# Optimization experiments

Measured on AMD Instinct MI355X. Metric: run time of the kernel, lower is better.

The kernel has to match this reference:

```python
import jax, jax.numpy as jnp
import numpy as np

B, S, D, H = 128, 512, 512, 4
DH = D // H

def setup_inputs() -> dict:
    key = jax.random.key(0)
    ks = jax.random.split(key, 12)
    s = 1.0 / np.sqrt(D)
    inp = {
        "x": jax.random.normal(ks[0], (B, S, D), dtype=jnp.float32),
        "Wi": jax.random.uniform(ks[1], (D, D), jnp.float32, -s, s),
        "bi": jnp.zeros((D,), jnp.float32),
        "Wq": jax.random.uniform(ks[2], (D, D), jnp.float32, -s, s),
        "bq": jnp.zeros((D,), jnp.float32),
        "Wk": jax.random.uniform(ks[3], (D, D), jnp.float32, -s, s),
        "bk": jnp.zeros((D,), jnp.float32),
        "Wv": jax.random.uniform(ks[4], (D, D), jnp.float32, -s, s),
        "bv": jnp.zeros((D,), jnp.float32),
        "Wo": jax.random.uniform(ks[5], (D, D), jnp.float32, -s, s),
        "bo": jnp.zeros((D,), jnp.float32),
        "data_lens": jax.random.randint(ks[6], (B,), 1, S + 1, dtype=jnp.int32),
    }
    return inp


def _forward(x, Wi, bi, Wq, bq, Wk, bk, Wv, bv, Wo, bo, data_lens):
    # fc_i applied to the whole sequence up front
    xf = x @ Wi + bi                      # [B, S, D]
    h0 = xf[:, 0, :]                      # initial state = fc_i(x)[:, 0]
    scale = 1.0 / jnp.sqrt(jnp.asarray(DH, xf.dtype))

    def step(h, x_t):
        # h: [B, D] previous state (acts as key and value, kv_len == 1)
        # x_t: [B, D] current input (query)
        q = (x_t @ Wq + bq).reshape(B, H, DH)
        k = (h @ Wk + bk).reshape(B, H, DH)
        v = (h @ Wv + bv).reshape(B, H, DH)
        scores = jnp.sum(q * k, axis=-1, keepdims=True) * scale   # [B, H, 1]
        w = jax.nn.softmax(scores, axis=-1)                       # == 1 (single key)
        attn = (w * v).reshape(B, D)
        h_new = attn @ Wo + bo + x_t                              # residual
        return h_new, h_new

    xs = jnp.transpose(xf, (1, 0, 2))     # [S, B, D]
    _, outs = jax.lax.scan(step, h0, xs)  # [S, B, D]
    outputs = jnp.transpose(outs, (1, 0, 2))                      # [B, S, D]

    idx = (data_lens.astype(jnp.int32) - 1)[:, None, None]        # [B,1,1]
    final_state = jnp.take_along_axis(outputs, idx, axis=1)[:, 0, :]
    return outputs, final_state


def reference(x, Wi, bi, Wq, bq, Wk, bk, Wv, bv, Wo, bo, data_lens):
    return _forward(x, Wi, bi, Wq, bq, Wk, bk, Wv, bv, Wo, bo, data_lens)
```

## Files before the change

kernel.cpp:

```cpp
#include <hip/hip_runtime.h>
#include <hip/hip_bf16.h>

typedef __hip_bfloat16 bf16;
typedef __attribute__((ext_vector_type(8))) short short8;
typedef __attribute__((ext_vector_type(4))) float f32x4;

#define S_LEN 512
#define DIM   512
#define BATCH 128
#define ROWS  (BATCH * S_LEN)

__device__ inline unsigned short f2bu(float f){
    bf16 h = __float2bfloat16(f);
    return *reinterpret_cast<unsigned short*>(&h);
}
__device__ inline float ld_in(const void* p, size_t i, int f32){
    return f32 ? ((const float*)p)[i] : __bfloat162float(((const bf16*)p)[i]);
}

typedef __attribute__((address_space(1))) const unsigned int gu32;
typedef __attribute__((address_space(3))) unsigned int lu32;
__device__ __forceinline__ void gld16(const void* g, void* l){
    __builtin_amdgcn_global_load_lds((gu32*)g, (lu32*)l, 16, 0, 0);
}

__global__ void detect_dtype(const unsigned int* __restrict__ x, int* __restrict__ flag)
{
    __shared__ int cnt;
    if (threadIdx.x == 0) cnt = 0;
    __syncthreads();
    int loc = 0;
    for (int i = threadIdx.x; i < 8192; i += 256)
        if (((x[i] >> 7) & 0xFFu) == 0xFFu) loc++;
    atomicAdd(&cnt, loc);
    __syncthreads();
    if (threadIdx.x == 0) *flag = (cnt > 0) ? 1 : 0;
}

__global__ void conv_tr(const void* __restrict__ in, bf16* __restrict__ outp,
                        const int* __restrict__ flagp)
{
    const int f32 = *flagp;
    __shared__ unsigned short tile[32][33];
    const int bx = blockIdx.x, by = blockIdx.y;
    const int tx = threadIdx.x, ty = threadIdx.y;
    #pragma unroll
    for (int j = 0; j < 32; j += 8)
        tile[ty + j][tx] = f2bu(ld_in(in, (size_t)(by*32 + ty + j)*DIM + bx*32 + tx, f32));
    __syncthreads();
    #pragma unroll
    for (int j = 0; j < 32; j += 8) {
        unsigned short u = tile[tx][ty + j];
        outp[(size_t)(bx*32 + ty + j)*DIM + by*32 + tx] = *reinterpret_cast<bf16*>(&u);
    }
}

__global__ void conv_cp(const void* __restrict__ in, bf16* __restrict__ outp,
                        const int* __restrict__ flagp)
{
    const int f32 = *flagp;
    const size_t i = (size_t)blockIdx.x*256 + threadIdx.x;
    outp[i] = __float2bfloat16(ld_in(in, i, f32));
}

__global__ void conv_x(const void* __restrict__ X, size_t eoff, bf16* __restrict__ xb,
                       const int* __restrict__ flagp)
{
    const int f32 = *flagp;
    const size_t i = ((size_t)blockIdx.x*256 + threadIdx.x)*8;
    if (f32) {
        const float* p = (const float*)X + eoff + i;
        float4 a = *(const float4*)p;
        float4 b = *(const float4*)(p + 4);
        __align__(16) unsigned short wv[8];
        wv[0]=f2bu(a.x); wv[1]=f2bu(a.y); wv[2]=f2bu(a.z); wv[3]=f2bu(a.w);
        wv[4]=f2bu(b.x); wv[5]=f2bu(b.y); wv[6]=f2bu(b.z); wv[7]=f2bu(b.w);
        *(uint4*)(xb + i) = *(const uint4*)wv;
    } else {
        *(uint4*)(xb + i) = *(const uint4*)((const bf16*)X + eoff + i);
    }
}

__global__ void cvec_kernel(const bf16* __restrict__ WoT, const void* __restrict__ bv,
                            const void* __restrict__ bo, const void* __restrict__ bi,
                            const int* __restrict__ flagp,
                            float* __restrict__ dvec, float* __restrict__ bvec)
{
    const int f32 = *flagp;
    const int n = blockIdx.x * 4 + (threadIdx.x >> 6);
    const int lane = threadIdx.x & 63;
    float acc = 0.f;
    for (int k = lane; k < DIM; k += 64)
        acc += ld_in(bv, k, f32) * __bfloat162float(WoT[(size_t)n*DIM + k]);
    #pragma unroll
    for (int o = 32; o > 0; o >>= 1) acc += __shfl_down(acc, o, 64);
    if (lane == 0) {
        const float dd = acc + ld_in(bo, n, f32);
        dvec[n] = dd;
        bvec[n] = dd + ld_in(bi, n, f32);
    }
}

__global__ void prep_aux(const float* __restrict__ U0, const float* __restrict__ V0,
                         const float* __restrict__ dvec,
                         bf16* __restrict__ A1, bf16* __restrict__ V0b, bf16* __restrict__ Zr)
{
    const int idx = blockIdx.x * 256 + threadIdx.x;
    const int n = idx & 511;
    A1[idx]  = __float2bfloat16(U0[idx] - dvec[n]);
    V0b[idx] = __float2bfloat16(V0[idx]);
    if (idx < 512) Zr[idx] = __float2bfloat16(0.f);
}

#define TILE_PROLOGUE                                                          \
    __shared__ __align__(16) unsigned short As[128][72];                       \
    __shared__ __align__(16) unsigned short Bs[128][72];                       \
    const int tid  = threadIdx.x;                                              \
    const int lane = tid & 63;                                                 \
    const int wave = tid >> 6;                                                 \
    const int wm = (wave & 1) * 64;                                            \
    const int wn = (wave >> 1) * 64;                                           \
    const int cn = lane & 15;                                                  \
    const int quad = lane >> 4;                                                \
    f32x4 acc[4][4];                                                           \
    _Pragma("unroll")                                                          \
    for (int i = 0; i < 4; ++i)                                                \
        _Pragma("unroll")                                                      \
        for (int j = 0; j < 4; ++j) acc[i][j] = (f32x4){0.f,0.f,0.f,0.f};

#define TILE_MFMA                                                              \
        __syncthreads();                                                       \
        _Pragma("unroll")                                                      \
        for (int ks = 0; ks < 64; ks += 32) {                                  \
            short8 af[4], bfr[4];                                              \
            const int koff = ks + quad*8;                                      \
            _Pragma("unroll")                                                  \
            for (int i = 0; i < 4; ++i) af[i]  = *(const short8*)&As[wm + i*16 + cn][koff]; \
            _Pragma("unroll")                                                  \
            for (int j = 0; j < 4; ++j) bfr[j] = *(const short8*)&Bs[wn + j*16 + cn][koff]; \
            _Pragma("unroll")                                                  \
            for (int i = 0; i < 4; ++i)                                        \
                _Pragma("unroll")                                              \
                for (int j = 0; j < 4; ++j)                                    \
                    acc[i][j] = __builtin_amdgcn_mfma_f32_16x16x32_bf16(af[i], bfr[j], acc[i][j], 0, 0, 0); \
        }                                                                      \
        __syncthreads();

#define STAGE_B(Bt, C0)                                                        \
        {                                                                      \
            int r = tid >> 3; const int c = (tid & 7) * 8;                     \
            _Pragma("unroll")                                                  \
            for (int p = 0; p < 4; ++p, r += 32) {                             \
                uint4 v = *(const uint4*)((Bt) + (size_t)((C0) + r)*DIM + k0 + c); \
                *(uint4*)&Bs[r][c] = v;                                        \
            }                                                                  \
        }

#define STAGE_A_IN(SRC, BASE)                                                  \
                if (f32) {                                                     \
                    const float* sp = (const float*)(SRC) + (BASE);            \
                    float4 a = *(const float4*)sp;                             \
                    float4 b = *(const float4*)(sp + 4);                       \
                    __align__(16) unsigned short w[8];                         \
                    w[0]=f2bu(a.x); w[1]=f2bu(a.y); w[2]=f2bu(a.z); w[3]=f2bu(a.w); \
                    w[4]=f2bu(b.x); w[5]=f2bu(b.y); w[6]=f2bu(b.z); w[7]=f2bu(b.w); \
                    *(uint4*)&As[r][c] = *(const uint4*)w;                     \
                } else {                                                       \
                    *(uint4*)&As[r][c] = *(const uint4*)((const bf16*)(SRC) + (BASE)); \
                }

__global__ __launch_bounds__(256) void gemm_sq(const bf16* __restrict__ A,
        const bf16* __restrict__ Btm, bf16* __restrict__ Pout, bf16* __restrict__ Tout)
{
    TILE_PROLOGUE
    const int R0 = blockIdx.y * 128;
    const int C0 = blockIdx.x * 128;
    for (int k0 = 0; k0 < DIM; k0 += 64) {
        {
            int r = tid >> 3; const int c = (tid & 7) * 8;
            #pragma unroll
            for (int p = 0; p < 4; ++p, r += 32)
                *(uint4*)&As[r][c] = *(const uint4*)(A + (size_t)(R0 + r)*DIM + k0 + c);
        }
        STAGE_B(Btm, C0)
        TILE_MFMA
    }
    #pragma unroll
    for (int i = 0; i < 4; ++i) {
        const int rowb = R0 + wm + i*16 + quad*4;
        #pragma unroll
        for (int j = 0; j < 4; ++j) {
            const int cc = C0 + wn + j*16 + cn;
            #pragma unroll
            for (int rr = 0; rr < 4; ++rr) {
                const float v = acc[i][j][rr];
                Pout[(size_t)(rowb + rr)*DIM + cc] = __float2bfloat16(v);
                Tout[(size_t)cc*DIM + rowb + rr]  = __float2bfloat16(v);
            }
        }
    }
}

__global__ __launch_bounds__(256) void gemm_row0(const void* __restrict__ X,
        const bf16* __restrict__ WiT, const float* __restrict__ bvec,
        const int* __restrict__ flagp, float* __restrict__ U0)
{
    const int f32 = *flagp;
    TILE_PROLOGUE
    const int C0 = blockIdx.x * 128;
    for (int k0 = 0; k0 < DIM; k0 += 64) {
        {
            int r = tid >> 3; const int c = (tid & 7) * 8;
            #pragma unroll
            for (int p = 0; p < 4; ++p, r += 32) {
                const size_t base = (size_t)r*S_LEN*DIM + k0 + c;
                STAGE_A_IN(X, base)
            }
        }
        STAGE_B(WiT, C0)
        TILE_MFMA
    }
    #pragma unroll
    for (int i = 0; i < 4; ++i) {
        const int rowb = wm + i*16 + quad*4;
        #pragma unroll
        for (int j = 0; j < 4; ++j) {
            const int cc = C0 + wn + j*16 + cn;
            const float bb = bvec[cc];
            #pragma unroll
            for (int rr = 0; rr < 4; ++rr)
                U0[(size_t)(rowb + rr)*DIM + cc] = acc[i][j][rr] + bb;
        }
    }
}

__global__ __launch_bounds__(256) void gemm_v0(const float* __restrict__ U0,
        const bf16* __restrict__ T0, const float* __restrict__ dvec, float* __restrict__ V0)
{
    TILE_PROLOGUE
    const int C0 = blockIdx.x * 128;
    for (int k0 = 0; k0 < DIM; k0 += 64) {
        {
            int r = tid >> 3; const int c = (tid & 7) * 8;
            #pragma unroll
            for (int p = 0; p < 4; ++p, r += 32) {
                __align__(16) unsigned short w[8];
                #pragma unroll
                for (int q = 0; q < 8; ++q)
                    w[q] = f2bu(U0[(size_t)r*DIM + k0 + c + q] - dvec[k0 + c + q]);
                *(uint4*)&As[r][c] = *(const uint4*)w;
            }
        }
        STAGE_B(T0, C0)
        TILE_MFMA
    }
    #pragma unroll
    for (int i = 0; i < 4; ++i) {
        const int rowb = wm + i*16 + quad*4;
        #pragma unroll
        for (int j = 0; j < 4; ++j) {
            const int cc = C0 + wn + j*16 + cn;
            #pragma unroll
            for (int rr = 0; rr < 4; ++rr) {
                const size_t off = (size_t)(rowb + rr)*DIM + cc;
                V0[off] = acc[i][j][rr] + U0[off];
            }
        }
    }
}

template<int MODE, bool TO_OUT>
__global__ __launch_bounds__(256) void gemm_big(
        const bf16* __restrict__ Abf, const bf16* __restrict__ A1,
        const bf16* __restrict__ V0b, const bf16* __restrict__ Zr,
        const bf16* __restrict__ Bt,  const float* __restrict__ Rf,
        float* __restrict__ Of, bf16* __restrict__ Ob,
        void* __restrict__ Oout, size_t eoff, const int* __restrict__ flagp,
        const int shift)
{
    __shared__ __align__(16) unsigned short As[128*64];
    __shared__ __align__(16) unsigned short Bs[128*64];
    const int tid  = threadIdx.x;
    const int lane = tid & 63;
    const int w    = tid >> 6;
    const int nb = gridDim.x;
    const int p0 = blockIdx.x;
    const int L  = (p0 & 7) * (nb >> 3) + (p0 >> 3);
    const int bx = L & 3, by = L >> 2;
    const int R0 = by * 128, C0 = bx * 128;
    const int wm = (w & 1) * 64;
    const int wn = (w >> 1) * 64;
    const int cn = lane & 15;
    const int quad = lane >> 4;
    f32x4 acc[4][4];
    #pragma unroll
    for (int i = 0; i < 4; ++i)
        #pragma unroll
        for (int j = 0; j < 4; ++j) acc[i][j] = (f32x4){0.f,0.f,0.f,0.f};

    const int lr = lane >> 3;
    const int lc = (lane & 7) * 8;
    const bf16* ab[4];
    const bf16* bb[4];
    #pragma unroll
    for (int p = 0; p < 4; ++p) {
        const int seg  = w*4 + p;
        const int r    = seg*8 + lr;
        const int grow = R0 + r;
        const bf16* a;
        if (MODE == 2) {
            a = Abf + (size_t)grow*DIM;
        } else if (MODE == 1) {
            const int t = grow & (S_LEN - 1);
            if      (t == 0) a = A1  + (size_t)(grow >> 9)*DIM;
            else if (t == 1) a = V0b + (size_t)(grow >> 9)*DIM;
            else             a = Abf + (size_t)(grow - 1)*DIM;
        } else {
            const int t = grow & (S_LEN - 1);
            a = (t >= shift) ? (Abf + (size_t)(grow - shift)*DIM) : Zr;
        }
        ab[p] = a + lc;
        bb[p] = Bt + (size_t)(C0 + r)*DIM + lc;
    }

    for (int k0 = 0; k0 < DIM; k0 += 64) {
        #pragma unroll
        for (int p = 0; p < 4; ++p) {
            const int seg = w*4 + p;
            gld16(ab[p] + k0, &As[seg*512]);
            gld16(bb[p] + k0, &Bs[seg*512]);
        }
        __syncthreads();
        #pragma unroll
        for (int ks = 0; ks < 64; ks += 32) {
            short8 af[4], bfr[4];
            const int koff = ks + quad*8;
            #pragma unroll
            for (int i = 0; i < 4; ++i) af[i]  = *(const short8*)&As[(wm + i*16 + cn)*64 + koff];
            #pragma unroll
            for (int j = 0; j < 4; ++j) bfr[j] = *(const short8*)&Bs[(wn + j*16 + cn)*64 + koff];
            #pragma unroll
            for (int i = 0; i < 4; ++i)
                #pragma unroll
                for (int j = 0; j < 4; ++j)
                    acc[i][j] = __builtin_amdgcn_mfma_f32_16x16x32_bf16(af[i], bfr[j], acc[i][j], 0, 0, 0);
        }
        __syncthreads();
    }

    const int f32o = TO_OUT ? *flagp : 0;
    #pragma unroll
    for (int i = 0; i < 4; ++i) {
        const int rowb = R0 + wm + i*16 + quad*4;
        #pragma unroll
        for (int j = 0; j < 4; ++j) {
            const int cc = C0 + wn + j*16 + cn;
            #pragma unroll
            for (int rr = 0; rr < 4; ++rr) {
                const size_t off = (size_t)(rowb + rr)*DIM + cc;
                const float res = (MODE == 2) ? Rf[cc] : Rf[off];
                const float v = acc[i][j][rr] + res;
                if (TO_OUT) {
                    if (f32o) ((float*)Oout)[eoff + off] = v;
                    else      ((bf16*)Oout)[eoff + off]  = __float2bfloat16(v);
                } else {
                    Of[off] = v;
                    Ob[off] = __float2bfloat16(v);
                }
            }
        }
    }
}

__global__ void gather_final(void* __restrict__ out, const int* __restrict__ lens,
                             const int* __restrict__ flagp)
{
    const int f32 = *flagp;
    const int idx = blockIdx.x * 256 + threadIdx.x;
    const int b = idx >> 9, n = idx & 511;
    int L = lens[b];
    if (L < 1) L = 1;
    if (L > S_LEN) L = S_LEN;
    const size_t src = ((size_t)b*S_LEN + (L - 1))*DIM + n;
    const size_t dst = (size_t)ROWS*DIM + idx;
    if (f32) ((float*)out)[dst] = ((const float*)out)[src];
    else     ((bf16*)out)[dst]  = ((const bf16*)out)[src];
}

extern "C" void kernel_launch(void* const* d_in, const int* in_sizes, int n_in,
                              void* d_out, int out_size, void* d_ws, size_t ws_size,
                              hipStream_t stream)
{
    const void* X  = d_in[0];
    const void* Wi = d_in[1];
    const void* bi = d_in[2];
    const void* Wv = d_in[7];
    const void* bv = d_in[8];
    const void* Wo = d_in[9];
    const void* bo = d_in[10];
    const int* lens = (const int*)d_in[11];
    char* ws = (char*)d_ws;

    const size_t MATB = (size_t)DIM * DIM * sizeof(bf16);
    bf16* WiT = (bf16*)(ws + 0*MATB);
    bf16* WoT = (bf16*)(ws + 1*MATB);
    bf16* Wvb = (bf16*)(ws + 2*MATB);
    bf16* S2  = (bf16*)(ws + 3*MATB);
    bf16* S3  = (bf16*)(ws + 4*MATB);
    bf16* T0  = (bf16*)(ws + 5*MATB);
    bf16* T1  = (bf16*)(ws + 6*MATB);
    bf16* T2  = (bf16*)(ws + 7*MATB);
    bf16* T3  = (bf16*)(ws + 8*MATB);
    size_t off = 9*MATB;
    float* dvec = (float*)(ws + off); off += 2048;
    float* bvec = (float*)(ws + off); off += 2048;
    int*   flag = (int*)  (ws + off); off += 256;
    float* U0   = (float*)(ws + off); off += (size_t)BATCH*DIM*4;
    float* V0   = (float*)(ws + off); off += (size_t)BATCH*DIM*4;
    bf16*  A1   = (bf16*) (ws + off); off += (size_t)BATCH*DIM*2;
    bf16*  V0b  = (bf16*) (ws + off); off += (size_t)BATCH*DIM*2;
    bf16*  Zr   = (bf16*) (ws + off); off += 1024;
    off = (off + 1023) & ~(size_t)1023;
    char* dyn = ws + off;
    const size_t avail = ws_size > off ? ws_size - off : 0;

    int CR = 512;
    for (long cr = 65536; cr >= 512; cr >>= 1)
        if ((size_t)cr * 7168 <= avail) { CR = (int)cr; break; }

    bf16*  xbf = (bf16*) dyn;
    float* Uf  = (float*)(dyn + (size_t)CR*1024);
    bf16*  Ub  = (bf16*) (dyn + (size_t)CR*3072);
    float* Vf  = (float*)(dyn + (size_t)CR*4096);
    bf16*  Vb  = (bf16*) (dyn + (size_t)CR*6144);

    detect_dtype<<<1, 256, 0, stream>>>((const unsigned int*)X, flag);
    conv_tr<<<dim3(16,16), dim3(32,8), 0, stream>>>(Wi, WiT, flag);
    conv_tr<<<dim3(16,16), dim3(32,8), 0, stream>>>(Wo, WoT, flag);
    conv_cp<<<1024, 256, 0, stream>>>(Wv, Wvb, flag);
    cvec_kernel<<<128, 256, 0, stream>>>(WoT, bv, bo, bi, flag, dvec, bvec);
    gemm_sq<<<dim3(4,4), 256, 0, stream>>>(Wvb, WoT, S2, T0);
    gemm_sq<<<dim3(4,4), 256, 0, stream>>>(S2, T0, S3, T1);
    gemm_sq<<<dim3(4,4), 256, 0, stream>>>(S3, T1, S2, T2);
    gemm_sq<<<dim3(4,4), 256, 0, stream>>>(S2, T2, S3, T3);
    gemm_row0<<<dim3(4,1), 256, 0, stream>>>(X, WiT, bvec, flag, U0);
    gemm_v0<<<dim3(4,1), 256, 0, stream>>>(U0, T0, dvec, V0);
    prep_aux<<<256, 256, 0, stream>>>(U0, V0, dvec, A1, V0b, Zr);

    const int NC = ROWS / CR;
    const int RT = CR / 128;
    const int nb = 4 * RT;
    for (int c = 0; c < NC; ++c) {
        const size_t eoff = (size_t)c*CR*DIM;
        const size_t boff = (size_t)(c*(CR/S_LEN))*DIM;
        conv_x<<<CR/4, 256, 0, stream>>>(X, eoff, xbf, flag);
        gemm_big<2,false><<<nb, 256, 0, stream>>>(xbf, nullptr, nullptr, Zr,
                WiT, bvec, Uf, Ub, nullptr, 0, flag, 0);
        gemm_big<1,false><<<nb, 256, 0, stream>>>(Ub, A1 + boff, V0b + boff, Zr,
                T0, Uf, Vf, Vb, nullptr, 0, flag, 1);
        gemm_big<0,false><<<nb, 256, 0, stream>>>(Vb, nullptr, nullptr, Zr,
                T1, Vf, Uf, Ub, nullptr, 0, flag, 2);
        gemm_big<0,false><<<nb, 256, 0, stream>>>(Ub, nullptr, nullptr, Zr,
                T2, Uf, Vf, Vb, nullptr, 0, flag, 4);
        gemm_big<0,true ><<<nb, 256, 0, stream>>>(Vb, nullptr, nullptr, Zr,
                T3, Vf, nullptr, nullptr, d_out, eoff, flag, 8);
    }
    gather_final<<<256, 256, 0, stream>>>(d_out, lens, flag);
}
```

Baseline: 1.029 ms.

## Double-buffer LDS tiles with XOR swizzle and interleaved prefetch in big GEMM

The big GEMM kernel now uses double-buffered LDS tiles. Global-to-LDS loads for the next K-tile are issued in four phases, each interleaved with a quarter of the MFMA work, with explicit vmcnt waits and barriers in place of the load-sync-compute-sync loop. LDS rows are XOR-swizzled to cut bank conflicts on fragment reads, setprio raises priority around the MFMAs, and launch bounds request two blocks per CU. The hand-placed waitcnts and barriers are delicate: doubled LDS (64KB) and the last-iteration wraparound prefetch add redundant traffic and possible occupancy or correctness risk.

```diff
diff --git a/kernel.cpp b/kernel.cpp
--- a/kernel.cpp
+++ b/kernel.cpp
@@ -22,6 +22,11 @@
 typedef __attribute__((address_space(3))) unsigned int lu32;
 __device__ __forceinline__ void gld16(const void* g, void* l){
     __builtin_amdgcn_global_load_lds((gu32*)g, (lu32*)l, 16, 0, 0);
+}
+
+__device__ __forceinline__ short8 lds_frag(const unsigned short* base, int row, int koff){
+    const unsigned off = ((unsigned)(row*128 + koff*2)) ^ (((unsigned)(row & 7)) << 4);
+    return *(const short8*)((const char*)base + off);
 }
 
 __global__ void detect_dtype(const unsigned int* __restrict__ x, int* __restrict__ flag)
@@ -270,7 +275,7 @@
 }
 
 template<int MODE, bool TO_OUT>
-__global__ __launch_bounds__(256) void gemm_big(
+__global__ __launch_bounds__(256, 2) void gemm_big(
         const bf16* __restrict__ Abf, const bf16* __restrict__ A1,
         const bf16* __restrict__ V0b, const bf16* __restrict__ Zr,
         const bf16* __restrict__ Bt,  const float* __restrict__ Rf,
@@ -278,8 +283,8 @@
         void* __restrict__ Oout, size_t eoff, const int* __restrict__ flagp,
         const int shift)
 {
-    __shared__ __align__(16) unsigned short As[128*64];
-    __shared__ __align__(16) unsigned short Bs[128*64];
+    __shared__ __align__(16) unsigned short As[2][128*64];
+    __shared__ __align__(16) unsigned short Bs[2][128*64];
     const int tid  = threadIdx.x;
     const int lane = tid & 63;
     const int w    = tid >> 6;
@@ -298,14 +303,13 @@
         #pragma unroll
         for (int j = 0; j < 4; ++j) acc[i][j] = (f32x4){0.f,0.f,0.f,0.f};
 
-    const int lr = lane >> 3;
-    const int lc = (lane & 7) * 8;
-    const bf16* ab[4];
-    const bf16* bb[4];
-    #pragma unroll
-    for (int p = 0; p < 4; ++p) {
-        const int seg  = w*4 + p;
-        const int r    = seg*8 + lr;
+    const int lr  = w*8 + (lane >> 3);
+    const int lcb = ((lane & 7) ^ (lane >> 3)) * 8;
+    const bf16* aln[4];
+    const bf16* bln[4];
+    #pragma unroll
+    for (int l = 0; l < 4; ++l) {
+        const int r    = l*32 + lr;
         const int grow = R0 + r;
         const bf16* a;
         if (MODE == 2) {
@@ -319,34 +323,70 @@
             const int t = grow & (S_LEN - 1);
             a = (t >= shift) ? (Abf + (size_t)(grow - shift)*DIM) : Zr;
         }
-        ab[p] = a + lc;
-        bb[p] = Bt + (size_t)(C0 + r)*DIM + lc;
-    }
-
-    for (int k0 = 0; k0 < DIM; k0 += 64) {
-        #pragma unroll
-        for (int p = 0; p < 4; ++p) {
-            const int seg = w*4 + p;
-            gld16(ab[p] + k0, &As[seg*512]);
-            gld16(bb[p] + k0, &Bs[seg*512]);
-        }
-        __syncthreads();
-        #pragma unroll
-        for (int ks = 0; ks < 64; ks += 32) {
-            short8 af[4], bfr[4];
-            const int koff = ks + quad*8;
-            #pragma unroll
-            for (int i = 0; i < 4; ++i) af[i]  = *(const short8*)&As[(wm + i*16 + cn)*64 + koff];
-            #pragma unroll
-            for (int j = 0; j < 4; ++j) bfr[j] = *(const short8*)&Bs[(wn + j*16 + cn)*64 + koff];
-            #pragma unroll
-            for (int i = 0; i < 4; ++i)
-                #pragma unroll
-                for (int j = 0; j < 4; ++j)
-                    acc[i][j] = __builtin_amdgcn_mfma_f32_16x16x32_bf16(af[i], bfr[j], acc[i][j], 0, 0, 0);
-        }
-        __syncthreads();
-    }
+        aln[l] = a + lcb;
+        bln[l] = Bt + (size_t)(C0 + r)*DIM + lcb;
+    }
+
+    {
+        unsigned short* Ad = &As[0][0];
+        unsigned short* Bd = &Bs[0][0];
+        gld16(aln[0], Ad + 0*2048 + w*512);
+        gld16(aln[2], Ad + 2*2048 + w*512);
+        gld16(bln[0], Bd + 0*2048 + w*512);
+        gld16(bln[2], Bd + 2*2048 + w*512);
+        gld16(aln[1], Ad + 1*2048 + w*512);
+        gld16(aln[3], Ad + 3*2048 + w*512);
+        gld16(bln[1], Bd + 1*2048 + w*512);
+        gld16(bln[3], Bd + 3*2048 + w*512);
+    }
+    asm volatile("s_waitcnt vmcnt(4)" ::: "memory");
+    __builtin_amdgcn_s_barrier();
+
+#define PHASE(MQ, NQ, STAGEA, L0, L1, DOWAIT)                                   \
+    {                                                                           \
+        short8 af0 = lds_frag(&As[cur][0], wm + (MQ)*32 +  0 + cn,      quad*8);\
+        short8 af1 = lds_frag(&As[cur][0], wm + (MQ)*32 + 16 + cn,      quad*8);\
+        short8 af2 = lds_frag(&As[cur][0], wm + (MQ)*32 +  0 + cn, 32 + quad*8);\
+        short8 af3 = lds_frag(&As[cur][0], wm + (MQ)*32 + 16 + cn, 32 + quad*8);\
+        short8 bg0 = lds_frag(&Bs[cur][0], wn + (NQ)*32 +  0 + cn,      quad*8);\
+        short8 bg1 = lds_frag(&Bs[cur][0], wn + (NQ)*32 + 16 + cn,      quad*8);\
+        short8 bg2 = lds_frag(&Bs[cur][0], wn + (NQ)*32 +  0 + cn, 32 + quad*8);\
+        short8 bg3 = lds_frag(&Bs[cur][0], wn + (NQ)*32 + 16 + cn, 32 + quad*8);\
+        if (STAGEA) {                                                           \
+            gld16(aln[L0] + knt, Ad + (L0)*2048 + w*512);                       \
+            gld16(aln[L1] + knt, Ad + (L1)*2048 + w*512);                       \
+        } else {                                                                \
+            gld16(bln[L0] + knt, Bd + (L0)*2048 + w*512);                       \
+            gld16(bln[L1] + knt, Bd + (L1)*2048 + w*512);                       \
+        }                                                                       \
+        __builtin_amdgcn_s_barrier();                                           \
+        __builtin_amdgcn_s_setprio(1);                                          \
+        acc[(MQ)*2+0][(NQ)*2+0] = __builtin_amdgcn_mfma_f32_16x16x32_bf16(af0, bg0, acc[(MQ)*2+0][(NQ)*2+0], 0, 0, 0); \
+        acc[(MQ)*2+1][(NQ)*2+0] = __builtin_amdgcn_mfma_f32_16x16x32_bf16(af1, bg0, acc[(MQ)*2+1][(NQ)*2+0], 0, 0, 0); \
+        acc[(MQ)*2+0][(NQ)*2+1] = __builtin_amdgcn_mfma_f32_16x16x32_bf16(af0, bg1, acc[(MQ)*2+0][(NQ)*2+1], 0, 0, 0); \
+        acc[(MQ)*2+1][(NQ)*2+1] = __builtin_amdgcn_mfma_f32_16x16x32_bf16(af1, bg1, acc[(MQ)*2+1][(NQ)*2+1], 0, 0, 0); \
+        acc[(MQ)*2+0][(NQ)*2+0] = __builtin_amdgcn_mfma_f32_16x16x32_bf16(af2, bg2, acc[(MQ)*2+0][(NQ)*2+0], 0, 0, 0); \
+        acc[(MQ)*2+1][(NQ)*2+0] = __builtin_amdgcn_mfma_f32_16x16x32_bf16(af3, bg2, acc[(MQ)*2+1][(NQ)*2+0], 0, 0, 0); \
+        acc[(MQ)*2+0][(NQ)*2+1] = __builtin_amdgcn_mfma_f32_16x16x32_bf16(af2, bg3, acc[(MQ)*2+0][(NQ)*2+1], 0, 0, 0); \
+        acc[(MQ)*2+1][(NQ)*2+1] = __builtin_amdgcn_mfma_f32_16x16x32_bf16(af3, bg3, acc[(MQ)*2+1][(NQ)*2+1], 0, 0, 0); \
+        __builtin_amdgcn_s_setprio(0);                                          \
+        if (DOWAIT) asm volatile("s_waitcnt vmcnt(4)" ::: "memory");            \
+        __builtin_amdgcn_s_barrier();                                           \
+    }
+
+    #pragma unroll
+    for (int kt = 0; kt < 8; ++kt) {
+        const int cur = kt & 1;
+        const int knt = ((kt + 1) & 7) * 64;
+        unsigned short* Ad = &As[cur ^ 1][0];
+        unsigned short* Bd = &Bs[cur ^ 1][0];
+        PHASE(0, 0, true,  0, 2, 1)
+        PHASE(1, 0, false, 0, 2, 1)
+        PHASE(0, 1, true,  1, 3, 0)
+        PHASE(1, 1, false, 1, 3, 1)
+    }
+#undef PHASE
+    asm volatile("s_waitcnt vmcnt(0)" ::: "memory");
 
     const int f32o = TO_OUT ? *flagp : 0;
     #pragma unroll
```

Result: no change. 1.016 ms (-1.2%).

## Double-buffer LDS with swizzled layout and 64-row tiles in big GEMM

Applied to the files above, without the earlier changes.

Rewrites the main GEMM's inner loop to double-buffer LDS tiles, so the global->LDS loads for the next k-step are issued before the MFMAs on the current one. It also XOR-swizzles the LDS layout to avoid bank conflicts and halves the row tile to 64, doubling the block count. It sets launch_bounds occupancy to 3 and raises wave priority around the MFMA section. The cost is more LDS per block, more blocks that each reuse less data, and a full vmcnt(0) wait plus a barrier every iteration.

```diff
diff --git a/kernel.cpp b/kernel.cpp
--- a/kernel.cpp
+++ b/kernel.cpp
@@ -22,6 +22,11 @@
 typedef __attribute__((address_space(3))) unsigned int lu32;
 __device__ __forceinline__ void gld16(const void* g, void* l){
     __builtin_amdgcn_global_load_lds((gu32*)g, (lu32*)l, 16, 0, 0);
+}
+
+__device__ __forceinline__ short8 lds_frag(const unsigned short* base, int row, int koff){
+    const unsigned off = ((unsigned)(row*128 + koff*2)) ^ (((unsigned)(row & 7)) << 4);
+    return *(const short8*)((const char*)base + off);
 }
 
 __global__ void detect_dtype(const unsigned int* __restrict__ x, int* __restrict__ flag)
@@ -270,7 +275,7 @@
 }
 
 template<int MODE, bool TO_OUT>
-__global__ __launch_bounds__(256) void gemm_big(
+__global__ __launch_bounds__(256, 3) void gemm_big(
         const bf16* __restrict__ Abf, const bf16* __restrict__ A1,
         const bf16* __restrict__ V0b, const bf16* __restrict__ Zr,
         const bf16* __restrict__ Bt,  const float* __restrict__ Rf,
@@ -278,8 +283,8 @@
         void* __restrict__ Oout, size_t eoff, const int* __restrict__ flagp,
         const int shift)
 {
-    __shared__ __align__(16) unsigned short As[128*64];
-    __shared__ __align__(16) unsigned short Bs[128*64];
+    __shared__ __align__(16) unsigned short As[2][64*64];
+    __shared__ __align__(16) unsigned short Bs[2][128*64];
     const int tid  = threadIdx.x;
     const int lane = tid & 63;
     const int w    = tid >> 6;
@@ -287,26 +292,25 @@
     const int p0 = blockIdx.x;
     const int L  = (p0 & 7) * (nb >> 3) + (p0 >> 3);
     const int bx = L & 3, by = L >> 2;
-    const int R0 = by * 128, C0 = bx * 128;
-    const int wm = (w & 1) * 64;
+    const int R0 = by * 64, C0 = bx * 128;
+    const int wm = (w & 1) * 32;
     const int wn = (w >> 1) * 64;
     const int cn = lane & 15;
     const int quad = lane >> 4;
-    f32x4 acc[4][4];
-    #pragma unroll
-    for (int i = 0; i < 4; ++i)
+    f32x4 acc[2][4];
+    #pragma unroll
+    for (int i = 0; i < 2; ++i)
         #pragma unroll
         for (int j = 0; j < 4; ++j) acc[i][j] = (f32x4){0.f,0.f,0.f,0.f};
 
-    const int lr = lane >> 3;
-    const int lc = (lane & 7) * 8;
-    const bf16* ab[4];
-    const bf16* bb[4];
-    #pragma unroll
-    for (int p = 0; p < 4; ++p) {
-        const int seg  = w*4 + p;
-        const int r    = seg*8 + lr;
-        const int grow = R0 + r;
+    const int lr  = w*8 + (lane >> 3);
+    const int lcb = ((lane & 7) ^ (lane >> 3)) * 8;
+    const int ldst = w * 512;
+    const bf16* aln[2];
+    const bf16* bln[4];
+    #pragma unroll
+    for (int l = 0; l < 2; ++l) {
+        const int grow = R0 + l*32 + lr;
         const bf16* a;
         if (MODE == 2) {
             a = Abf + (size_t)grow*DIM;
@@ -319,38 +323,58 @@
             const int t = grow & (S_LEN - 1);
             a = (t >= shift) ? (Abf + (size_t)(grow - shift)*DIM) : Zr;
         }
-        ab[p] = a + lc;
-        bb[p] = Bt + (size_t)(C0 + r)*DIM + lc;
-    }
-
-    for (int k0 = 0; k0 < DIM; k0 += 64) {
-        #pragma unroll
-        for (int p = 0; p < 4; ++p) {
-            const int seg = w*4 + p;
-            gld16(ab[p] + k0, &As[seg*512]);
-            gld16(bb[p] + k0, &Bs[seg*512]);
-        }
-        __syncthreads();
-        #pragma unroll
-        for (int ks = 0; ks < 64; ks += 32) {
-            short8 af[4], bfr[4];
-            const int koff = ks + quad*8;
-            #pragma unroll
-            for (int i = 0; i < 4; ++i) af[i]  = *(const short8*)&As[(wm + i*16 + cn)*64 + koff];
-            #pragma unroll
-            for (int j = 0; j < 4; ++j) bfr[j] = *(const short8*)&Bs[(wn + j*16 + cn)*64 + koff];
-            #pragma unroll
-            for (int i = 0; i < 4; ++i)
-                #pragma unroll
-                for (int j = 0; j < 4; ++j)
-                    acc[i][j] = __builtin_amdgcn_mfma_f32_16x16x32_bf16(af[i], bfr[j], acc[i][j], 0, 0, 0);
-        }
-        __syncthreads();
-    }
+        aln[l] = a + lcb;
+    }
+    #pragma unroll
+    for (int l = 0; l < 4; ++l)
+        bln[l] = Bt + (size_t)(C0 + l*32 + lr)*DIM + lcb;
+
+#define STAGE(BUF, KN)                                                         \
+    {                                                                          \
+        gld16(aln[0] + (KN), &As[BUF][0*2048 + ldst]);                         \
+        gld16(aln[1] + (KN), &As[BUF][1*2048 + ldst]);                         \
+        gld16(bln[0] + (KN), &Bs[BUF][0*2048 + ldst]);                         \
+        gld16(bln[1] + (KN), &Bs[BUF][1*2048 + ldst]);                         \
+        gld16(bln[2] + (KN), &Bs[BUF][2*2048 + ldst]);                         \
+        gld16(bln[3] + (KN), &Bs[BUF][3*2048 + ldst]);                         \
+    }
+
+    STAGE(0, 0)
+    asm volatile("s_waitcnt vmcnt(0)" ::: "memory");
+    __builtin_amdgcn_s_barrier();
+
+    #pragma unroll
+    for (int kt = 0; kt < 8; ++kt) {
+        const int cur = kt & 1;
+        if (kt < 7) STAGE(cur ^ 1, (kt + 1) * 64)
+        short8 af[2][2], bfr[4][2];
+        #pragma unroll
+        for (int i = 0; i < 2; ++i) {
+            af[i][0] = lds_frag(&As[cur][0], wm + i*16 + cn,      quad*8);
+            af[i][1] = lds_frag(&As[cur][0], wm + i*16 + cn, 32 + quad*8);
+        }
+        #pragma unroll
+        for (int j = 0; j < 4; ++j) {
+            bfr[j][0] = lds_frag(&Bs[cur][0], wn + j*16 + cn,      quad*8);
+            bfr[j][1] = lds_frag(&Bs[cur][0], wn + j*16 + cn, 32 + quad*8);
+        }
+        __builtin_amdgcn_s_setprio(1);
+        #pragma unroll
+        for (int i = 0; i < 2; ++i)
+            #pragma unroll
+            for (int j = 0; j < 4; ++j) {
+                acc[i][j] = __builtin_amdgcn_mfma_f32_16x16x32_bf16(af[i][0], bfr[j][0], acc[i][j], 0, 0, 0);
+                acc[i][j] = __builtin_amdgcn_mfma_f32_16x16x32_bf16(af[i][1], bfr[j][1], acc[i][j], 0, 0, 0);
+            }
+        __builtin_amdgcn_s_setprio(0);
+        asm volatile("s_waitcnt vmcnt(0)" ::: "memory");
+        __builtin_amdgcn_s_barrier();
+    }
+#undef STAGE
 
     const int f32o = TO_OUT ? *flagp : 0;
     #pragma unroll
-    for (int i = 0; i < 4; ++i) {
+    for (int i = 0; i < 2; ++i) {
         const int rowb = R0 + wm + i*16 + quad*4;
         #pragma unroll
         for (int j = 0; j < 4; ++j) {
@@ -448,8 +472,7 @@
     prep_aux<<<256, 256, 0, stream>>>(U0, V0, dvec, A1, V0b, Zr);
 
     const int NC = ROWS / CR;
-    const int RT = CR / 128;
-    const int nb = 4 * RT;
+    const int nb = (CR / 64) * 4;
     for (int c = 0; c < NC; ++c) {
         const size_t eoff = (size_t)c*CR*DIM;
         const size_t boff = (size_t)(c*(CR/S_LEN))*DIM;
```

After: 963.7 us. 6.3% less time.
